# Kernel optimization log

Hardware: AMD Instinct MI355X
Metric: run time of the kernel (lower is better)

Reference implementation:

```python
import jax, jax.numpy as jnp
from jax import lax
import numpy as np


def _conv4d(x, w, b, stride, padding):
    # Faithful 4D conv emulation: K temporal slices, each its own 3D conv.
    # x: [B,Ci,T,D,H,W]; w: [K,Co,Ci,k,k,k]; b: [K,Co] or None.
    # Quirk preserved: bias b[i] is added once per contributing temporal tap i
    # (the torch code accumulates full conv3d outputs including bias).
    B, Ci, T = x.shape[0], x.shape[1], x.shape[2]
    K = w.shape[0]
    O = (T + 2 * padding - K) // stride + 1
    out = None
    for i in range(K):
        j = np.arange(O) * stride + i - padding          # static input frame idx per output frame
        valid = (j >= 0) & (j < T)
        jc = np.clip(j, 0, T - 1)
        xg = jnp.moveaxis(x[:, :, jc], 2, 1)             # [B,O,Ci,D,H,W]
        xg = xg.reshape(B * O, Ci, x.shape[3], x.shape[4], x.shape[5])
        y = lax.conv_general_dilated(xg, w[i], (stride,) * 3, [(padding, padding)] * 3,
                                     dimension_numbers=('NCDHW', 'OIDHW', 'NCDHW'))
        if b is not None:
            y = y + b[i][None, :, None, None, None]
        y = y.reshape(B, O, y.shape[1], y.shape[2], y.shape[3], y.shape[4])
        y = y * jnp.asarray(valid, y.dtype)[None, :, None, None, None, None]
        out = y if out is None else out + y
    return jnp.moveaxis(out, 1, 2)                       # [B,Co,O,D',H',W']


def _maxpool4d(x, k, s, p):
    # pool3d-per-frame then pool1d over T == one 4D max pool (max commutes)
    return lax.reduce_window(x, jnp.array(-jnp.inf, x.dtype), lax.max,
                             (1, 1, k, k, k, k), (1, 1, s, s, s, s),
                             [(0, 0), (0, 0)] + [(p, p)] * 4)


def _avgpool4d_2(x):
    # avg-of-avgs over a full (2,2,2,2) window == 4D average
    s = lax.reduce_window(x, jnp.array(0.0, x.dtype), lax.add,
                          (1, 1, 2, 2, 2, 2), (1,) * 6, [(0, 0)] * 6)
    return s / jnp.asarray(16.0, x.dtype)


def _block(x, w1, b1, w2, b2, stride, dw):
    y = jax.nn.relu(_conv4d(x, w1, b1, stride, 1))
    y = _conv4d(y, w2, b2, 1, 1)
    res = x if dw is None else _conv4d(x, dw, None, stride, 0)
    return jax.nn.relu(y + res)


def _forward(x, conv1_w, l1_w1, l1_b1, l1_w2, l1_b2,
             l2_w1, l2_b1, l2_w2, l2_b2, l2_dw,
             l3_w1, l3_b1, l3_w2, l3_b2, l3_dw,
             l4_w1, l4_b1, l4_w2, l4_b2, l4_dw, fc_w, fc_b):
    h = x[:, None]                                       # [B,1,T,D,H,W]
    h = jax.nn.relu(_conv4d(h, conv1_w, None, 2, 3))     # 36 -> 18
    h = _maxpool4d(h, 3, 2, 1)                           # 18 -> 9
    h = _block(h, l1_w1, l1_b1, l1_w2, l1_b2, 1, None)   # 9
    h = _block(h, l2_w1, l2_b1, l2_w2, l2_b2, 2, l2_dw)  # 9 -> 5
    h = _block(h, l3_w1, l3_b1, l3_w2, l3_b2, 2, l3_dw)  # 5 -> 3
    h = _block(h, l4_w1, l4_b1, l4_w2, l4_b2, 2, l4_dw)  # 3 -> 2
    h = _avgpool4d_2(h)                                  # 2 -> 1
    h = h.reshape(-1, 512)
    return h @ fc_w.T + fc_b


def setup_inputs() -> dict:
    key = jax.random.key(0)
    ks = jax.random.split(key, 40)
    ctr = iter(range(40))
    def w(shape, fan):
        return jax.random.normal(ks[next(ctr)], shape, jnp.float32) * np.float32(np.sqrt(2.0 / fan))
    def bias(shape):
        return jax.random.normal(ks[next(ctr)], shape, jnp.float32) * np.float32(0.01)
    d = {}
    d['x'] = jax.random.normal(ks[next(ctr)], (1, 36, 36, 36, 36), jnp.float32)
    d['conv1_w'] = w((7, 64, 1, 7, 7, 7), 343)
    d['l1_w1'] = w((3, 64, 64, 3, 3, 3), 64 * 27); d['l1_b1'] = bias((3, 64))
    d['l1_w2'] = w((3, 64, 64, 3, 3, 3), 64 * 27); d['l1_b2'] = bias((3, 64))
    d['l2_w1'] = w((3, 128, 64, 3, 3, 3), 64 * 27); d['l2_b1'] = bias((3, 128))
    d['l2_w2'] = w((3, 128, 128, 3, 3, 3), 128 * 27); d['l2_b2'] = bias((3, 128))
    d['l2_dw'] = w((1, 128, 64, 1, 1, 1), 64)
    d['l3_w1'] = w((3, 256, 128, 3, 3, 3), 128 * 27); d['l3_b1'] = bias((3, 256))
    d['l3_w2'] = w((3, 256, 256, 3, 3, 3), 256 * 27); d['l3_b2'] = bias((3, 256))
    d['l3_dw'] = w((1, 256, 128, 1, 1, 1), 128)
    d['l4_w1'] = w((3, 512, 256, 3, 3, 3), 256 * 27); d['l4_b1'] = bias((3, 512))
    d['l4_w2'] = w((3, 512, 512, 3, 3, 3), 512 * 27); d['l4_b2'] = bias((3, 512))
    d['l4_dw'] = w((1, 512, 256, 1, 1, 1), 256)
    d['fc_w'] = w((1, 512), 512); d['fc_b'] = bias((1,))
    return d


def reference(x, conv1_w, l1_w1, l1_b1, l1_w2, l1_b2,
              l2_w1, l2_b1, l2_w2, l2_b2, l2_dw,
              l3_w1, l3_b1, l3_w2, l3_b2, l3_dw,
              l4_w1, l4_b1, l4_w2, l4_b2, l4_dw, fc_w, fc_b):
    return _forward(x, conv1_w, l1_w1, l1_b1, l1_w2, l1_b2,
                    l2_w1, l2_b1, l2_w2, l2_b2, l2_dw,
                    l3_w1, l3_b1, l3_w2, l3_b2, l3_dw,
                    l4_w1, l4_b1, l4_w2, l4_b2, l4_dw, fc_w, fc_b)
```

## Files before the change

### kernel.cpp

```cpp
#include <hip/hip_runtime.h>

typedef __bf16 bf16x8 __attribute__((ext_vector_type(8)));
typedef float f32x4 __attribute__((ext_vector_type(4)));
typedef unsigned short ushortT;

__device__ __forceinline__ unsigned short f2bf(float f) {
    unsigned u = __float_as_uint(f);
    u += 0x7fffu + ((u >> 16) & 1u);
    return (unsigned short)(u >> 16);
}
__device__ __forceinline__ float bf2f(unsigned short h) {
    return __uint_as_float((unsigned)h << 16);
}

__global__ __launch_bounds__(256) void prep0(const float* __restrict__ x,
                                             const float* __restrict__ c1w,
                                             const float* __restrict__ w11, const float* __restrict__ w12,
                                             const float* __restrict__ w21, const float* __restrict__ w22,
                                             const float* __restrict__ w31, const float* __restrict__ w32,
                                             const float* __restrict__ w41, const float* __restrict__ w42,
                                             ushortT* __restrict__ xp,
                                             ushortT* __restrict__ o1,
                                             ushortT* __restrict__ o11, ushortT* __restrict__ o12,
                                             ushortT* __restrict__ o21, ushortT* __restrict__ o22,
                                             ushortT* __restrict__ o31, ushortT* __restrict__ o32,
                                             ushortT* __restrict__ o41, ushortT* __restrict__ o42) {
    __shared__ float tile[6960];
    int bid = blockIdx.x, tid = threadIdx.x;
    if (bid < 1737) {
        long idx = (long)bid * 256 + tid;
        if (idx >= 444528L) return;
        int q = (int)(idx % 6); long r = idx / 6;
        int h = (int)(r % 42); r /= 42;
        int d = (int)(r % 42); int t = (int)(r / 42);
        int tt = t - 3, dd = d - 3, hh = h - 3;
        bool rok = ((unsigned)tt < 36u) && ((unsigned)dd < 36u) && ((unsigned)hh < 36u);
        const float* src = x + (((long)tt * 36 + dd) * 36 + hh) * 36;
        union { ushortT s[8]; uint4 u; } v;
#pragma unroll
        for (int j = 0; j < 8; ++j) {
            int ww = q * 8 + j - 3;
            float f = (rok && (unsigned)ww < 36u) ? src[ww] : 0.f;
            v.s[j] = f2bf(f);
        }
        *(uint4*)(xp + idx * 8) = v.u;
        return;
    }
    if (bid < 2521) {
        int e = (bid - 1737) * 256 + tid;
        if (e < 200704) {
            int k = e % 3136, co = e / 3136;
            int kw = k & 7, kh = (k >> 3) & 7, kdt = k >> 6;
            int kt = kdt / 7, kd = kdt % 7;
            float v = 0.f;
            if (kh < 7 && kw < 7)
                v = c1w[(size_t)(kt * 64 + co) * 343 + kd * 49 + kh * 7 + kw];
            o1[e] = f2bf(v);
        }
        return;
    }

    int wb = bid - 2521;
    const float* in; ushortT* out; int Ci, Co;
    int base;
    if (wb < 192) {
        if (wb < 48) {
            if (wb < 24) { in = w11; out = o11; Ci = 64; Co = 64; base = 0; }
            else         { in = w12; out = o12; Ci = 64; Co = 64; base = 24; }
        } else if (wb < 96) { in = w21; out = o21; Ci = 64;  Co = 128; base = 48; }
        else                { in = w22; out = o22; Ci = 128; Co = 128; base = 96; }
    } else if (wb < 768) {
        if (wb < 384) { in = w31; out = o31; Ci = 128; Co = 256; base = 192; }
        else          { in = w32; out = o32; Ci = 256; Co = 256; base = 384; }
    } else {
        if (wb < 1536) { in = w41; out = o41; Ci = 256; Co = 512; base = 768; }
        else           { in = w42; out = o42; Ci = 512; Co = 512; base = 1536; }
    }
    int lb = wb - base;
    int nCb = Co >> 4, nKb = Ci >> 5;
    int per_i = nCb * nKb;
    int i = lb / per_i;
    int r2 = lb - i * per_i;
    int cb = r2 / nKb, kb = r2 - cb * nKb;

    size_t costride = (size_t)Ci * 27;
    ushortT* dst0 = out + (((size_t)(i * 27) * nCb + cb) * nKb + kb) * 512;
    size_t tapstride = (size_t)nCb * nKb * 512;

    for (int ph = 0; ph < 2; ++ph) {
        const float* src0 = in + ((size_t)(i * Co + cb * 16) * Ci + kb * 32 + ph * 16) * 27;
        for (int e = tid; e < 1728; e += 256) {
            int cl = e / 108, q = e - cl * 108;
            *(float4*)(tile + cl * 435 + 4 * q) = *(const float4*)(src0 + cl * costride + 4 * q);
        }
        __syncthreads();
        for (int e = tid; e < 864; e += 256) {
            int tap = e >> 5, wl = e & 31;
            int gh = wl >> 4, l15 = wl & 15;
            union { ushortT s[8]; uint4 u; } v;
#pragma unroll
            for (int j = 0; j < 8; ++j)
                v.s[j] = f2bf(tile[l15 * 435 + (gh * 8 + j) * 27 + tap]);
            *(uint4*)(dst0 + (size_t)tap * tapstride + (ph * 32 + wl) * 8) = v.u;
        }
        __syncthreads();
    }
}

__global__ __launch_bounds__(128) void mega_kernel(
        const ushortT* __restrict__ xp, const ushortT* __restrict__ aw,
        ushortT* __restrict__ outc1) {
    __shared__ __align__(16) ushortT smem[12376];
    int bid = blockIdx.x, tid = threadIdx.x;

    {
        int xcd = bid & 7, loc = bid >> 3;
        bid = (xcd < 6) ? (xcd * 169 + loc) : (1014 + (xcd - 6) * 168 + loc);
    }

    int wt = bid % 5; int r = bid / 5;
    int ht = r % 5; r /= 5;
    int dt = r % 3; int ot = r / 3;
    int ow0 = wt * 4, oh0 = ht * 4, od0 = dt * 6;
    int gw0 = 2 * ow0, gh0 = 2 * oh0, gd0 = 2 * od0;

    int lane = tid & 63, wv = tid >> 6;
    int l15 = lane & 15, g = lane >> 4;
    int dh = l15 >> 2, dw = l15 & 3;

    const ushortT* ap0 = aw + (size_t)(wv * 32 + l15) * 3136 + g * 8;
    const ushortT* ap1 = ap0 + 16 * 3136;

    ushortT* curb = smem;
    ushortT* nxtb = smem + 6188;

    auto stage = [&](ushortT* buf, int kt) {
        int gt = 2 * ot + kt;
        for (int rr = tid; rr < 238; rr += 128) {
            int ld = rr / 14, lh = rr - ld * 14;
            const ushortT* s = xp +
                ((size_t)((gt * 42 + gd0 + ld) * 42 + gh0 + lh)) * 48 + gw0;
            uint4 a = *(const uint4*)s;
            uint4 b = *(const uint4*)(s + 8);
            unsigned* d = (unsigned*)buf + rr * 13;
            d[0] = a.x; d[1] = a.y; d[2] = a.z; d[3] = a.w;
            d[4] = b.x; d[5] = b.y; d[6] = b.z; d[7] = b.w;
        }
    };

    f32x4 acc[2][6];
#pragma unroll
    for (int c = 0; c < 2; ++c)
#pragma unroll
        for (int m = 0; m < 6; ++m) acc[c][m] = (f32x4){0.f, 0.f, 0.f, 0.f};

    stage(curb, 0);
    __syncthreads();

    int lhl = (2 * dh + g) * 26 + 2 * dw;
    int kidx = 0;
    for (int kt = 0; kt < 7; ++kt) {
        if (kt < 6) stage(nxtb, kt + 1);
        for (int kd = 0; kd < 7; ++kd) {
            int C0 = kd * 364 + lhl;
#pragma unroll
            for (int khq = 0; khq < 2; ++khq) {
                bf16x8 a0 = *(const bf16x8*)(ap0 + kidx);
                bf16x8 a1 = *(const bf16x8*)(ap1 + kidx);
                kidx += 32;
                int C = C0 + khq * 104;
#pragma unroll
                for (int m = 0; m < 6; ++m) {
                    int off = C + m * 728;
                    union { unsigned u[4]; bf16x8 v; } bb;
                    bb.u[0] = *(const unsigned*)(curb + off);
                    bb.u[1] = *(const unsigned*)(curb + off + 2);
                    bb.u[2] = *(const unsigned*)(curb + off + 4);
                    bb.u[3] = *(const unsigned*)(curb + off + 6);
                    acc[0][m] = __builtin_amdgcn_mfma_f32_16x16x32_bf16(a0, bb.v, acc[0][m], 0, 0, 0);
                    acc[1][m] = __builtin_amdgcn_mfma_f32_16x16x32_bf16(a1, bb.v, acc[1][m], 0, 0, 0);
                }
            }
        }
        __syncthreads();
        ushortT* t2 = curb; curb = nxtb; nxtb = t2;
    }

    int oh = oh0 + dh, ow = ow0 + dw;
    if (oh < 18 && ow < 18) {
#pragma unroll
        for (int m = 0; m < 6; ++m) {
            int od = od0 + m;
            int pos = ((ot * 18 + od) * 18 + oh) * 18 + ow;
#pragma unroll
            for (int c = 0; c < 2; ++c) {
                ushort4 st;
                st.x = f2bf(fmaxf(acc[c][m][0], 0.f));
                st.y = f2bf(fmaxf(acc[c][m][1], 0.f));
                st.z = f2bf(fmaxf(acc[c][m][2], 0.f));
                st.w = f2bf(fmaxf(acc[c][m][3], 0.f));
                *(ushort4*)(outc1 + (size_t)pos * 64 + wv * 32 + c * 16 + g * 4) = st;
            }
        }
    }
}

__global__ void maxpool2(const ushortT* __restrict__ in, ushortT* __restrict__ out,
                         ushortT* __restrict__ zb) {
    int idx = blockIdx.x * 256 + threadIdx.x;
    if (idx < 128) zb[idx] = 0;
    if (idx >= 6561 * 16) return;
    int c4 = idx & 15;
    int p = idx >> 4;
    int ow = p % 9; int t = p / 9;
    int oh = t % 9; t /= 9;
    int od = t % 9; int ot = t / 9;
    ushort4 m = {0, 0, 0, 0};
    for (int kt = 0; kt < 3; ++kt) { int it = 2 * ot + kt - 1; if ((unsigned)it >= 18u) continue;
        for (int kd = 0; kd < 3; ++kd) { int id = 2 * od + kd - 1; if ((unsigned)id >= 18u) continue;
            for (int kh = 0; kh < 3; ++kh) { int ih = 2 * oh + kh - 1; if ((unsigned)ih >= 18u) continue;
                int rb = ((it * 18 + id) * 18 + ih) * 18;
                for (int kw = 0; kw < 3; ++kw) { int iw = 2 * ow + kw - 1; if ((unsigned)iw >= 18u) continue;
                    ushort4 v = *(const ushort4*)(in + (size_t)(rb + iw) * 64 + c4 * 4);
                    m.x = v.x > m.x ? v.x : m.x;
                    m.y = v.y > m.y ? v.y : m.y;
                    m.z = v.z > m.z ? v.z : m.z;
                    m.w = v.w > m.w ? v.w : m.w;
                }
            }
        }
    }
    *(ushort4*)(out + (size_t)p * 64 + c4 * 4) = m;
}

template <int KC, int FUSE, int TS>
__global__ void convmfma(const ushortT* __restrict__ xb, const ushortT* __restrict__ wt,
                         const float* __restrict__ bias, const ushortT* __restrict__ res,
                         ushortT* __restrict__ outb, float* __restrict__ part,
                         const ushortT* __restrict__ zq,
                         int Ci, int Co, int T, int O, int stride, int chunk,
                         const float* __restrict__ dwW, ushortT* __restrict__ dwOut) {
    if (dwW && blockIdx.y == (unsigned)(Co >> 6)) {
        int O2 = O * O, O3 = O2 * O, O4 = O3 * O;
        int total = Co * O4;
        int sthr = gridDim.x * gridDim.z * 256;
        for (int idx = (blockIdx.z * gridDim.x + blockIdx.x) * 256 + threadIdx.x;
             idx < total; idx += sthr) {
            int co = idx % Co;
            int pos = idx / Co;
            int ow = pos % O, oh = (pos / O) % O, od = (pos / O2) % O, ot = pos / O3;
            int ip = (((2 * ot) * T + 2 * od) * T + 2 * oh) * T + 2 * ow;
            const ushortT* xpp = xb + (size_t)ip * Ci;
            const float* wp = dwW + (size_t)co * Ci;
            float acc = 0.f;
            for (int c8 = 0; c8 < Ci; c8 += 8) {
                uint4 xv = *(const uint4*)(xpp + c8);
                float4 w0 = *(const float4*)(wp + c8);
                float4 w1 = *(const float4*)(wp + c8 + 4);
                acc = fmaf(bf2f((unsigned short)(xv.x & 0xffff)), w0.x, acc);
                acc = fmaf(bf2f((unsigned short)(xv.x >> 16)),    w0.y, acc);
                acc = fmaf(bf2f((unsigned short)(xv.y & 0xffff)), w0.z, acc);
                acc = fmaf(bf2f((unsigned short)(xv.y >> 16)),    w0.w, acc);
                acc = fmaf(bf2f((unsigned short)(xv.z & 0xffff)), w1.x, acc);
                acc = fmaf(bf2f((unsigned short)(xv.z >> 16)),    w1.y, acc);
                acc = fmaf(bf2f((unsigned short)(xv.w & 0xffff)), w1.z, acc);
                acc = fmaf(bf2f((unsigned short)(xv.w >> 16)),    w1.w, acc);
            }
            dwOut[idx] = f2bf(acc);
        }
        return;
    }

    int lane = threadIdx.x & 63;
    int wv = threadIdx.x >> 6;
    int p0 = blockIdx.x * 16;
    int cb = blockIdx.y * 4 + wv;
    int co0 = cb * 16;
    int zz = blockIdx.z;
    int ks, ts;
    if (TS > 1) { ks = zz / TS; ts = zz % TS; } else { ks = zz; ts = 0; }
    int cbase = ks * chunk;
    int kb0 = cbase >> 5;
    size_t nCb = Co >> 4, nKb = Ci >> 5;

    int pn = p0 + (lane & 15);
    int O2 = O * O, O3 = O2 * O, O4 = O3 * O;
    bool pv = pn < O4;
    int pc = pv ? pn : 0;
    int ow = pc % O, oh = (pc / O) % O, od = (pc / O2) % O, ot = pc / O3;
    int g = lane >> 4;
    int kl = cbase + g * 8;

    const ushortT* zp = zq + g * 8;

    f32x4 acc[4];
#pragma unroll
    for (int a = 0; a < 4; ++a) acc[a] = (f32x4){0.f, 0.f, 0.f, 0.f};

    int itb = ot * stride - 1, idb = od * stride - 1, ihb = oh * stride - 1, iwb = ow * stride - 1;

    if (TS == 1) {
#pragma unroll
        for (int i = 0; i < 3; ++i) {
            int it = itb + i;
            bool vt = pv && ((unsigned)it < (unsigned)T);
#pragma unroll
            for (int kd = 0; kd < 3; ++kd) {
                int id = idb + kd;
                bool vdd = vt && ((unsigned)id < (unsigned)T);
                int btd = (it * T + id) * T;
#pragma unroll
                for (int kh = 0; kh < 3; ++kh) {
                    int ih = ihb + kh;
                    bool vh = vdd && ((unsigned)ih < (unsigned)T);
#pragma unroll
                    for (int kw = 0; kw < 3; ++kw) {
                        int iw = iwb + kw;
                        bool v = vh && ((unsigned)iw < (unsigned)T);
                        int ip = (btd + ih) * T + iw;
                        const int tap = (i * 9 + kd * 3 + kh) * 3 + kw;
                        const ushortT* bp = v ? (xb + (size_t)ip * Ci + kl) : zp;
                        const ushortT* ap = wt + (((size_t)tap * nCb + cb) * nKb + kb0) * 512
                                            + lane * 8;
#pragma unroll
                        for (int kc = 0; kc < KC; ++kc) {
                            bf16x8 av = *(const bf16x8*)(ap + kc * 512);
                            bf16x8 bv = *(const bf16x8*)(bp + kc * 32);
                            acc[(tap * KC + kc) & 3] =
                                __builtin_amdgcn_mfma_f32_16x16x32_bf16(av, bv,
                                    acc[(tap * KC + kc) & 3], 0, 0, 0);
                        }
                    }
                }
            }
        }
    } else {
        int i = ts / 3, kd = ts % 3;
        int it = itb + i;
        int id = idb + kd;
        bool vt = pv && ((unsigned)it < (unsigned)T) && ((unsigned)id < (unsigned)T);
        int btd = (it * T + id) * T;
        int tapb = i * 27 + kd * 9;
#pragma unroll
        for (int kh = 0; kh < 3; ++kh) {
            int ih = ihb + kh;
            bool vh = vt && ((unsigned)ih < (unsigned)T);
#pragma unroll
            for (int kw = 0; kw < 3; ++kw) {
                int iw = iwb + kw;
                bool v = vh && ((unsigned)iw < (unsigned)T);
                int ip = (btd + ih) * T + iw;
                int tap = tapb + kh * 3 + kw;
                const ushortT* bp = v ? (xb + (size_t)ip * Ci + kl) : zp;
                const ushortT* ap = wt + (((size_t)tap * nCb + cb) * nKb + kb0) * 512
                                    + lane * 8;
#pragma unroll
                for (int kc = 0; kc < KC; ++kc) {
                    bf16x8 av = *(const bf16x8*)(ap + kc * 512);
                    bf16x8 bv = *(const bf16x8*)(bp + kc * 32);
                    acc[(kh * 3 + kw + kc) & 3] =
                        __builtin_amdgcn_mfma_f32_16x16x32_bf16(av, bv,
                            acc[(kh * 3 + kw + kc) & 3], 0, 0, 0);
                }
            }
        }
    }

    if (!pv) return;
    f32x4 asum;
#pragma unroll
    for (int r = 0; r < 4; ++r)
        asum[r] = (acc[0][r] + acc[1][r]) + (acc[2][r] + acc[3][r]);
    int cob = co0 + g * 4;
    if (FUSE) {
        float bb[4] = {0.f, 0.f, 0.f, 0.f};
        for (int i = 0; i < 3; ++i) {
            int it = itb + i;
            if ((unsigned)it < (unsigned)T) {
#pragma unroll
                for (int rr = 0; rr < 4; ++rr) bb[rr] += bias[i * Co + cob + rr];
            }
        }
        float rv[4] = {0.f, 0.f, 0.f, 0.f};
        if (res) {
            ushort4 r4 = *(const ushort4*)(res + (size_t)pn * Co + cob);
            rv[0] = bf2f(r4.x); rv[1] = bf2f(r4.y); rv[2] = bf2f(r4.z); rv[3] = bf2f(r4.w);
        }
        ushort4 st;
        st.x = f2bf(fmaxf(asum[0] + bb[0] + rv[0], 0.f));
        st.y = f2bf(fmaxf(asum[1] + bb[1] + rv[1], 0.f));
        st.z = f2bf(fmaxf(asum[2] + bb[2] + rv[2], 0.f));
        st.w = f2bf(fmaxf(asum[3] + bb[3] + rv[3], 0.f));
        *(ushort4*)(outb + (size_t)pn * Co + cob) = st;
    } else {
        *(f32x4*)(part + ((size_t)zz * O4 + pn) * Co + cob) = asum;
    }
}

__global__ void finalize_k(const float* __restrict__ part, int KS,
                           const float* __restrict__ bias, const ushortT* __restrict__ res,
                           ushortT* __restrict__ outb, int Co, int O4, int T, int O, int stride,
                           int total) {
    int idx = blockIdx.x * 256 + threadIdx.x;
    if (idx >= total) return;
    int co = idx % Co;
    int pos = idx / Co;
    float v = 0.f;
    for (int z = 0; z < KS; ++z) v += part[((size_t)z * O4 + pos) * Co + co];
    int ot = pos / (O * O * O);
    for (int i = 0; i < 3; ++i) {
        int it = ot * stride + i - 1;
        if ((unsigned)it < (unsigned)T) v += bias[i * Co + co];
    }
    if (res) v += bf2f(res[idx]);
    outb[idx] = f2bf(fmaxf(v, 0.f));
}

__global__ void avgfc2(const ushortT* __restrict__ xin, const float* __restrict__ fw,
                       const float* __restrict__ fb, float* __restrict__ out) {
    __shared__ float ls[8];
    int t = threadIdx.x;
    float s = 0.f;
#pragma unroll
    for (int pp = 0; pp < 16; ++pp) s += bf2f(xin[pp * 512 + t]);
    s = s * (1.f / 16.f) * fw[t];
    for (int off = 32; off > 0; off >>= 1) s += __shfl_xor(s, off, 64);
    if ((t & 63) == 0) ls[t >> 6] = s;
    __syncthreads();
    if (t == 0) {
        float tot = 0.f;
#pragma unroll
        for (int i = 0; i < 8; ++i) tot += ls[i];
        out[0] = tot + fb[0];
    }
}

extern "C" void kernel_launch(void* const* d_in, const int* in_sizes, int n_in,
                              void* d_out, int out_size, void* d_ws, size_t ws_size,
                              hipStream_t stream) {
    const float* x       = (const float*)d_in[0];
    const float* conv1_w = (const float*)d_in[1];
    const float* l1_w1 = (const float*)d_in[2];
    const float* l1_b1 = (const float*)d_in[3];
    const float* l1_w2 = (const float*)d_in[4];
    const float* l1_b2 = (const float*)d_in[5];
    const float* l2_w1 = (const float*)d_in[6];
    const float* l2_b1 = (const float*)d_in[7];
    const float* l2_w2 = (const float*)d_in[8];
    const float* l2_b2 = (const float*)d_in[9];
    const float* l2_dw = (const float*)d_in[10];
    const float* l3_w1 = (const float*)d_in[11];
    const float* l3_b1 = (const float*)d_in[12];
    const float* l3_w2 = (const float*)d_in[13];
    const float* l3_b2 = (const float*)d_in[14];
    const float* l3_dw = (const float*)d_in[15];
    const float* l4_w1 = (const float*)d_in[16];
    const float* l4_b1 = (const float*)d_in[17];
    const float* l4_w2 = (const float*)d_in[18];
    const float* l4_b2 = (const float*)d_in[19];
    const float* l4_dw = (const float*)d_in[20];
    const float* fc_w  = (const float*)d_in[21];
    const float* fc_b  = (const float*)d_in[22];
    float* outp = (float*)d_out;

    char* bp = (char*)d_ws;
    auto alloc = [&](size_t bytes) {
        char* r = bp;
        bp += (bytes + 255) & ~(size_t)255;
        return (void*)r;
    };
    ushortT* A16 = (ushortT*)alloc(6718464ull * 2);
    ushortT* XP  = (ushortT*)alloc(3556224ull * 2);
    ushortT* Aw1 = (ushortT*)alloc(200704ull * 2);
    ushortT* X0 = (ushortT*)alloc(419904ull * 2);
    ushortT* Y1 = (ushortT*)alloc(419904ull * 2);
    ushortT* X1 = (ushortT*)alloc(419904ull * 2);
    ushortT* Y2 = (ushortT*)alloc(80000ull * 2);
    ushortT* R2 = (ushortT*)alloc(80000ull * 2);
    ushortT* X2 = (ushortT*)alloc(80000ull * 2);
    ushortT* Y3 = (ushortT*)alloc(20736ull * 2);
    ushortT* R3 = (ushortT*)alloc(20736ull * 2);
    ushortT* X3 = (ushortT*)alloc(20736ull * 2);
    ushortT* Y4 = (ushortT*)alloc(8192ull * 2);
    ushortT* R4 = (ushortT*)alloc(8192ull * 2);
    ushortT* X4 = (ushortT*)alloc(8192ull * 2);
    ushortT* W11 = (ushortT*)alloc(331776ull * 2);
    ushortT* W12 = (ushortT*)alloc(331776ull * 2);
    ushortT* W21 = (ushortT*)alloc(663552ull * 2);
    ushortT* W22 = (ushortT*)alloc(1327104ull * 2);
    ushortT* W31 = (ushortT*)alloc(2654208ull * 2);
    ushortT* W32 = (ushortT*)alloc(5308416ull * 2);
    ushortT* W41 = (ushortT*)alloc(10616832ull * 2);
    ushortT* W42 = (ushortT*)alloc(21233664ull * 2);
    float* P    = (float*)alloc(1492992ull * 4);
    ushortT* ZB = (ushortT*)alloc(256);
    if ((size_t)(bp - (char*)d_ws) > ws_size) return;

    prep0<<<5593, 256, 0, stream>>>(x, conv1_w,
                                    l1_w1, l1_w2, l2_w1, l2_w2, l3_w1, l3_w2, l4_w1, l4_w2,
                                    XP, Aw1,
                                    W11, W12, W21, W22, W31, W32, W41, W42);

    mega_kernel<<<1350, 128, 0, stream>>>(XP, Aw1, A16);

    maxpool2<<<411, 256, 0, stream>>>(A16, X0, ZB);

    convmfma<2, 1, 1><<<dim3(411, 1, 1), 256, 0, stream>>>(
        X0, W11, l1_b1, nullptr, Y1, nullptr, ZB, 64, 64, 9, 9, 1, 64, nullptr, nullptr);
    convmfma<2, 1, 1><<<dim3(411, 1, 1), 256, 0, stream>>>(
        Y1, W12, l1_b2, X0, X1, nullptr, ZB, 64, 64, 9, 9, 1, 64, nullptr, nullptr);

    convmfma<2, 1, 1><<<dim3(40, 3, 1), 256, 0, stream>>>(
        X1, W21, l2_b1, nullptr, Y2, nullptr, ZB, 64, 128, 9, 5, 2, 64, l2_dw, R2);
    convmfma<4, 1, 1><<<dim3(40, 2, 1), 256, 0, stream>>>(
        Y2, W22, l2_b2, R2, X2, nullptr, ZB, 128, 128, 5, 5, 1, 128, nullptr, nullptr);

    convmfma<1, 0, 9><<<dim3(6, 5, 36), 256, 0, stream>>>(
        X2, W31, nullptr, nullptr, nullptr, P, ZB, 128, 256, 5, 3, 2, 32, l3_dw, R3);
    finalize_k<<<81, 256, 0, stream>>>(P, 36, l3_b1, nullptr, Y3, 256, 81, 5, 3, 2, 20736);
    convmfma<1, 0, 9><<<dim3(6, 4, 72), 256, 0, stream>>>(
        Y3, W32, nullptr, nullptr, nullptr, P, ZB, 256, 256, 3, 3, 1, 32, nullptr, nullptr);
    finalize_k<<<81, 256, 0, stream>>>(P, 72, l3_b2, R3, X3, 256, 81, 3, 3, 1, 20736);

    convmfma<1, 0, 9><<<dim3(1, 9, 72), 256, 0, stream>>>(
        X3, W41, nullptr, nullptr, nullptr, P, ZB, 256, 512, 3, 2, 2, 32, l4_dw, R4);
    finalize_k<<<32, 256, 0, stream>>>(P, 72, l4_b1, nullptr, Y4, 512, 16, 3, 2, 2, 8192);
    convmfma<1, 0, 9><<<dim3(1, 8, 144), 256, 0, stream>>>(
        Y4, W42, nullptr, nullptr, nullptr, P, ZB, 512, 512, 2, 2, 1, 32, nullptr, nullptr);
    finalize_k<<<32, 256, 0, stream>>>(P, 144, l4_b2, R4, X4, 512, 16, 2, 2, 1, 8192);

    avgfc2<<<1, 512, 0, stream>>>(X4, fc_w, fc_b, outp);
}
```

Measured before the change: 474.7 us.

## Remove split-K partial sums and finalize kernels from deep conv layers

Drops the tap/channel split-K path that wrote fp32 partials for layers 3 and 4 and summed them in separate finalize kernels. Every conv now does its full reduction in one block and applies bias, residual and ReLU in its epilogue, with larger KC values for the deep layers. This removes four launches and the partial-buffer round trip through memory. In exchange, the deep layers run on very few blocks (as few as 8) that each do a long serial reduction, which risks leaving most of the GPU idle and exposing load latency.

```diff
diff --git a/kernel.cpp b/kernel.cpp
--- a/kernel.cpp
+++ b/kernel.cpp
@@ -233,12 +233,11 @@
     *(ushort4*)(out + (size_t)p * 64 + c4 * 4) = m;
 }
 
-template <int KC, int FUSE, int TS>
+template <int KC>
 __global__ void convmfma(const ushortT* __restrict__ xb, const ushortT* __restrict__ wt,
                          const float* __restrict__ bias, const ushortT* __restrict__ res,
-                         ushortT* __restrict__ outb, float* __restrict__ part,
-                         const ushortT* __restrict__ zq,
-                         int Ci, int Co, int T, int O, int stride, int chunk,
+                         ushortT* __restrict__ outb, const ushortT* __restrict__ zq,
+                         int Ci, int Co, int T, int O, int stride,
                          const float* __restrict__ dwW, ushortT* __restrict__ dwOut) {
     if (dwW && blockIdx.y == (unsigned)(Co >> 6)) {
         int O2 = O * O, O3 = O2 * O, O4 = O3 * O;
@@ -276,11 +275,6 @@
     int p0 = blockIdx.x * 16;
     int cb = blockIdx.y * 4 + wv;
     int co0 = cb * 16;
-    int zz = blockIdx.z;
-    int ks, ts;
-    if (TS > 1) { ks = zz / TS; ts = zz % TS; } else { ks = zz; ts = 0; }
-    int cbase = ks * chunk;
-    int kb0 = cbase >> 5;
     size_t nCb = Co >> 4, nKb = Ci >> 5;
 
     int pn = p0 + (lane & 15);
@@ -289,7 +283,7 @@
     int pc = pv ? pn : 0;
     int ow = pc % O, oh = (pc / O) % O, od = (pc / O2) % O, ot = pc / O3;
     int g = lane >> 4;
-    int kl = cbase + g * 8;
+    int kl = g * 8;
 
     const ushortT* zp = zq + g * 8;
 
@@ -299,71 +293,36 @@
 
     int itb = ot * stride - 1, idb = od * stride - 1, ihb = oh * stride - 1, iwb = ow * stride - 1;
 
-    if (TS == 1) {
-#pragma unroll
-        for (int i = 0; i < 3; ++i) {
-            int it = itb + i;
-            bool vt = pv && ((unsigned)it < (unsigned)T);
-#pragma unroll
-            for (int kd = 0; kd < 3; ++kd) {
-                int id = idb + kd;
-                bool vdd = vt && ((unsigned)id < (unsigned)T);
-                int btd = (it * T + id) * T;
-#pragma unroll
-                for (int kh = 0; kh < 3; ++kh) {
-                    int ih = ihb + kh;
-                    bool vh = vdd && ((unsigned)ih < (unsigned)T);
-#pragma unroll
-                    for (int kw = 0; kw < 3; ++kw) {
-                        int iw = iwb + kw;
-                        bool v = vh && ((unsigned)iw < (unsigned)T);
-                        int ip = (btd + ih) * T + iw;
-                        const int tap = (i * 9 + kd * 3 + kh) * 3 + kw;
-                        const ushortT* bp = v ? (xb + (size_t)ip * Ci + kl) : zp;
-                        const ushortT* ap = wt + (((size_t)tap * nCb + cb) * nKb + kb0) * 512
-                                            + lane * 8;
-#pragma unroll
-                        for (int kc = 0; kc < KC; ++kc) {
-                            bf16x8 av = *(const bf16x8*)(ap + kc * 512);
-                            bf16x8 bv = *(const bf16x8*)(bp + kc * 32);
-                            acc[(tap * KC + kc) & 3] =
-                                __builtin_amdgcn_mfma_f32_16x16x32_bf16(av, bv,
-                                    acc[(tap * KC + kc) & 3], 0, 0, 0);
-                        }
+    for (int i = 0; i < 3; ++i) {
+        int it = itb + i;
+        bool vt = pv && ((unsigned)it < (unsigned)T);
+        for (int kd = 0; kd < 3; ++kd) {
+            int id = idb + kd;
+            bool vdd = vt && ((unsigned)id < (unsigned)T);
+            int btd = (it * T + id) * T;
+            for (int kh = 0; kh < 3; ++kh) {
+                int ih = ihb + kh;
+                bool vh = vdd && ((unsigned)ih < (unsigned)T);
+                int tap0 = (i * 9 + kd * 3 + kh) * 3;
+#pragma unroll
+                for (int kw = 0; kw < 3; ++kw) {
+                    int iw = iwb + kw;
+                    bool v = vh && ((unsigned)iw < (unsigned)T);
+                    int ip = (btd + ih) * T + iw;
+                    const ushortT* bp = v ? (xb + (size_t)ip * Ci + kl) : zp;
+                    const ushortT* ap = wt + (((size_t)(tap0 + kw) * nCb + cb) * nKb) * 512
+                                        + lane * 8;
+#pragma unroll
+                    for (int kc = 0; kc < KC; ++kc) {
+                        bf16x8 av = *(const bf16x8*)(ap + kc * 512);
+                        bf16x8 bv = *(const bf16x8*)(bp + kc * 32);
+                        acc[(kw * KC + kc) & 3] =
+                            __builtin_amdgcn_mfma_f32_16x16x32_bf16(av, bv,
+                                acc[(kw * KC + kc) & 3], 0, 0, 0);
                     }
                 }
             }
         }
-    } else {
-        int i = ts / 3, kd = ts % 3;
-        int it = itb + i;
-        int id = idb + kd;
-        bool vt = pv && ((unsigned)it < (unsigned)T) && ((unsigned)id < (unsigned)T);
-        int btd = (it * T + id) * T;
-        int tapb = i * 27 + kd * 9;
-#pragma unroll
-        for (int kh = 0; kh < 3; ++kh) {
-            int ih = ihb + kh;
-            bool vh = vt && ((unsigned)ih < (unsigned)T);
-#pragma unroll
-            for (int kw = 0; kw < 3; ++kw) {
-                int iw = iwb + kw;
-                bool v = vh && ((unsigned)iw < (unsigned)T);
-                int ip = (btd + ih) * T + iw;
-                int tap = tapb + kh * 3 + kw;
-                const ushortT* bp = v ? (xb + (size_t)ip * Ci + kl) : zp;
-                const ushortT* ap = wt + (((size_t)tap * nCb + cb) * nKb + kb0) * 512
-                                    + lane * 8;
-#pragma unroll
-                for (int kc = 0; kc < KC; ++kc) {
-                    bf16x8 av = *(const bf16x8*)(ap + kc * 512);
-                    bf16x8 bv = *(const bf16x8*)(bp + kc * 32);
-                    acc[(kh * 3 + kw + kc) & 3] =
-                        __builtin_amdgcn_mfma_f32_16x16x32_bf16(av, bv,
-                            acc[(kh * 3 + kw + kc) & 3], 0, 0, 0);
-                }
-            }
-        }
     }
 
     if (!pv) return;
@@ -372,48 +331,25 @@
     for (int r = 0; r < 4; ++r)
         asum[r] = (acc[0][r] + acc[1][r]) + (acc[2][r] + acc[3][r]);
     int cob = co0 + g * 4;
-    if (FUSE) {
-        float bb[4] = {0.f, 0.f, 0.f, 0.f};
-        for (int i = 0; i < 3; ++i) {
-            int it = itb + i;
-            if ((unsigned)it < (unsigned)T) {
-#pragma unroll
-                for (int rr = 0; rr < 4; ++rr) bb[rr] += bias[i * Co + cob + rr];
-            }
-        }
-        float rv[4] = {0.f, 0.f, 0.f, 0.f};
-        if (res) {
-            ushort4 r4 = *(const ushort4*)(res + (size_t)pn * Co + cob);
-            rv[0] = bf2f(r4.x); rv[1] = bf2f(r4.y); rv[2] = bf2f(r4.z); rv[3] = bf2f(r4.w);
-        }
-        ushort4 st;
-        st.x = f2bf(fmaxf(asum[0] + bb[0] + rv[0], 0.f));
-        st.y = f2bf(fmaxf(asum[1] + bb[1] + rv[1], 0.f));
-        st.z = f2bf(fmaxf(asum[2] + bb[2] + rv[2], 0.f));
-        st.w = f2bf(fmaxf(asum[3] + bb[3] + rv[3], 0.f));
-        *(ushort4*)(outb + (size_t)pn * Co + cob) = st;
-    } else {
-        *(f32x4*)(part + ((size_t)zz * O4 + pn) * Co + cob) = asum;
-    }
-}
-
-__global__ void finalize_k(const float* __restrict__ part, int KS,
-                           const float* __restrict__ bias, const ushortT* __restrict__ res,
-                           ushortT* __restrict__ outb, int Co, int O4, int T, int O, int stride,
-                           int total) {
-    int idx = blockIdx.x * 256 + threadIdx.x;
-    if (idx >= total) return;
-    int co = idx % Co;
-    int pos = idx / Co;
-    float v = 0.f;
-    for (int z = 0; z < KS; ++z) v += part[((size_t)z * O4 + pos) * Co + co];
-    int ot = pos / (O * O * O);
+    float bb[4] = {0.f, 0.f, 0.f, 0.f};
     for (int i = 0; i < 3; ++i) {
-        int it = ot * stride + i - 1;
-        if ((unsigned)it < (unsigned)T) v += bias[i * Co + co];
-    }
-    if (res) v += bf2f(res[idx]);
-    outb[idx] = f2bf(fmaxf(v, 0.f));
+        int it = itb + i;
+        if ((unsigned)it < (unsigned)T) {
+#pragma unroll
+            for (int rr = 0; rr < 4; ++rr) bb[rr] += bias[i * Co + cob + rr];
+        }
+    }
+    float rv[4] = {0.f, 0.f, 0.f, 0.f};
+    if (res) {
+        ushort4 r4 = *(const ushort4*)(res + (size_t)pn * Co + cob);
+        rv[0] = bf2f(r4.x); rv[1] = bf2f(r4.y); rv[2] = bf2f(r4.z); rv[3] = bf2f(r4.w);
+    }
+    ushort4 st;
+    st.x = f2bf(fmaxf(asum[0] + bb[0] + rv[0], 0.f));
+    st.y = f2bf(fmaxf(asum[1] + bb[1] + rv[1], 0.f));
+    st.z = f2bf(fmaxf(asum[2] + bb[2] + rv[2], 0.f));
+    st.w = f2bf(fmaxf(asum[3] + bb[3] + rv[3], 0.f));
+    *(ushort4*)(outb + (size_t)pn * Co + cob) = st;
 }
 
 __global__ void avgfc2(const ushortT* __restrict__ xin, const float* __restrict__ fw,
@@ -492,7 +428,6 @@
     ushortT* W32 = (ushortT*)alloc(5308416ull * 2);
     ushortT* W41 = (ushortT*)alloc(10616832ull * 2);
     ushortT* W42 = (ushortT*)alloc(21233664ull * 2);
-    float* P    = (float*)alloc(1492992ull * 4);
     ushortT* ZB = (ushortT*)alloc(256);
     if ((size_t)(bp - (char*)d_ws) > ws_size) return;
 
@@ -505,29 +440,25 @@
 
     maxpool2<<<411, 256, 0, stream>>>(A16, X0, ZB);
 
-    convmfma<2, 1, 1><<<dim3(411, 1, 1), 256, 0, stream>>>(
-        X0, W11, l1_b1, nullptr, Y1, nullptr, ZB, 64, 64, 9, 9, 1, 64, nullptr, nullptr);
-    convmfma<2, 1, 1><<<dim3(411, 1, 1), 256, 0, stream>>>(
-        Y1, W12, l1_b2, X0, X1, nullptr, ZB, 64, 64, 9, 9, 1, 64, nullptr, nullptr);
-
-    convmfma<2, 1, 1><<<dim3(40, 3, 1), 256, 0, stream>>>(
-        X1, W21, l2_b1, nullptr, Y2, nullptr, ZB, 64, 128, 9, 5, 2, 64, l2_dw, R2);
-    convmfma<4, 1, 1><<<dim3(40, 2, 1), 256, 0, stream>>>(
-        Y2, W22, l2_b2, R2, X2, nullptr, ZB, 128, 128, 5, 5, 1, 128, nullptr, nullptr);
-
-    convmfma<1, 0, 9><<<dim3(6, 5, 36), 256, 0, stream>>>(
-        X2, W31, nullptr, nullptr, nullptr, P, ZB, 128, 256, 5, 3, 2, 32, l3_dw, R3);
-    finalize_k<<<81, 256, 0, stream>>>(P, 36, l3_b1, nullptr, Y3, 256, 81, 5, 3, 2, 20736);
-    convmfma<1, 0, 9><<<dim3(6, 4, 72), 256, 0, stream>>>(
-        Y3, W32, nullptr, nullptr, nullptr, P, ZB, 256, 256, 3, 3, 1, 32, nullptr, nullptr);
-    finalize_k<<<81, 256, 0, stream>>>(P, 72, l3_b2, R3, X3, 256, 81, 3, 3, 1, 20736);
-
-    convmfma<1, 0, 9><<<dim3(1, 9, 72), 256, 0, stream>>>(
-        X3, W41, nullptr, nullptr, nullptr, P, ZB, 256, 512, 3, 2, 2, 32, l4_dw, R4);
-    finalize_k<<<32, 256, 0, stream>>>(P, 72, l4_b1, nullptr, Y4, 512, 16, 3, 2, 2, 8192);
-    convmfma<1, 0, 9><<<dim3(1, 8, 144), 256, 0, stream>>>(
-        Y4, W42, nullptr, nullptr, nullptr, P, ZB, 512, 512, 2, 2, 1, 32, nullptr, nullptr);
-    finalize_k<<<32, 256, 0, stream>>>(P, 144, l4_b2, R4, X4, 512, 16, 2, 2, 1, 8192);
+    convmfma<2><<<dim3(411, 1, 1), 256, 0, stream>>>(
+        X0, W11, l1_b1, nullptr, Y1, ZB, 64, 64, 9, 9, 1, nullptr, nullptr);
+    convmfma<2><<<dim3(411, 1, 1), 256, 0, stream>>>(
+        Y1, W12, l1_b2, X0, X1, ZB, 64, 64, 9, 9, 1, nullptr, nullptr);
+
+    convmfma<2><<<dim3(40, 3, 1), 256, 0, stream>>>(
+        X1, W21, l2_b1, nullptr, Y2, ZB, 64, 128, 9, 5, 2, l2_dw, R2);
+    convmfma<4><<<dim3(40, 2, 1), 256, 0, stream>>>(
+        Y2, W22, l2_b2, R2, X2, ZB, 128, 128, 5, 5, 1, nullptr, nullptr);
+
+    convmfma<4><<<dim3(6, 5, 1), 256, 0, stream>>>(
+        X2, W31, l3_b1, nullptr, Y3, ZB, 128, 256, 5, 3, 2, l3_dw, R3);
+    convmfma<8><<<dim3(6, 4, 1), 256, 0, stream>>>(
+        Y3, W32, l3_b2, R3, X3, ZB, 256, 256, 3, 3, 1, nullptr, nullptr);
+
+    convmfma<8><<<dim3(4, 9, 1), 256, 0, stream>>>(
+        X3, W41, l4_b1, nullptr, Y4, ZB, 256, 512, 3, 2, 2, l4_dw, R4);
+    convmfma<16><<<dim3(1, 8, 1), 256, 0, stream>>>(
+        Y4, W42, l4_b2, R4, X4, ZB, 512, 512, 2, 2, 1, nullptr, nullptr);
 
     avgfc2<<<1, 512, 0, stream>>>(X4, fc_w, fc_b, outp);
 }
```

New measurement: 887.2 us. +86.9%, slower.
